# Kernel tuning notes

Hardware: AMD Instinct MI355X
Metric: run time of the kernel (lower is better)

## Reference

```python
import jax, jax.numpy as jnp
import numpy as np

H = 200          # LSTM hidden size
POOL = 16        # maxout pool size


def lstm_step(x, h, c, Wih, Whh, bih, bhh):
    # PyTorch LSTM gate order: i, f, g, o
    gates = x @ Wih.T + h @ Whh.T + bih + bhh  # [4H]
    i, f, g, o = jnp.split(gates, 4)
    i, f, o = jax.nn.sigmoid(i), jax.nn.sigmoid(f), jax.nn.sigmoid(o)
    g = jnp.tanh(g)
    c_new = f * c + i * g
    h_new = o * jnp.tanh(c_new)
    return h_new, c_new


def hmn(U, h, s, e, w1, w2, b2, w3, b3, w4, b4):
    T = U.shape[0]
    r = jnp.tanh(jnp.concatenate([h, s, e]) @ w1.T)                 # [200]
    x = jnp.concatenate([U, jnp.broadcast_to(r, (T, H))], axis=1)    # [T,600]
    m1 = jnp.max((x @ w2.T + b2).reshape(T, POOL, H), axis=1)        # [T,200]
    m2 = jnp.max((m1 @ w3.T + b3).reshape(T, POOL, H), axis=1)       # [T,200]
    a = jnp.max((jnp.concatenate([m1, m2], axis=1) @ w4.T + b4).reshape(T, POOL, 1), axis=1)
    return a[:, 0]                                                   # [T]


def decoder_fwd(U, lstm_Wih, lstm_Whh, lstm_bih, lstm_bhh,
                s_fc1w, s_fc2w, s_fc2b, s_fc3w, s_fc3b, s_fc4w, s_fc4b,
                e_fc1w, e_fc2w, e_fc2b, e_fc3w, e_fc3b, e_fc4w, e_fc4b):
    sp = (s_fc1w, s_fc2w, s_fc2b, s_fc3w, s_fc3b, s_fc4w, s_fc4b)
    ep = (e_fc1w, e_fc2w, e_fc2b, e_fc3w, e_fc3b, e_fc4w, e_fc4b)
    h = jnp.zeros(H, U.dtype)
    c = jnp.zeros(H, U.dtype)
    start = jnp.array(0)
    end = jnp.array(0)

    # iteration 0
    x = jnp.concatenate([U[start], U[end]])
    h, c = lstm_step(x, h, c, lstm_Wih, lstm_Whh, lstm_bih, lstm_bhh)
    alpha = hmn(U, h, U[start], U[end], *sp)
    beta = hmn(U, h, U[start], U[end], *ep)
    start, end = jnp.argmax(alpha), jnp.argmax(beta)
    alphas, betas = [alpha], [beta]
    done = jnp.array(False)

    # iterations 1..3 with early-exit freeze (original breaks when start/end converge)
    for _ in range(3):
        x = jnp.concatenate([U[start], U[end]])
        ch, cc = lstm_step(x, h, c, lstm_Wih, lstm_Whh, lstm_bih, lstm_bhh)
        ca = hmn(U, ch, U[start], U[end], *sp)
        cb = hmn(U, ch, U[start], U[end], *ep)
        ns, ne = jnp.argmax(ca), jnp.argmax(cb)
        alphas.append(jnp.where(done, alphas[-1], ca))
        betas.append(jnp.where(done, betas[-1], cb))
        new_done = done | ((ns == start) & (ne == end))
        h = jnp.where(done, h, ch)
        c = jnp.where(done, c, cc)
        start = jnp.where(done, start, ns)
        end = jnp.where(done, end, ne)
        done = new_done

    return jnp.stack(alphas), jnp.stack(betas)  # each [4, T]


def setup_inputs() -> dict:
    key = jax.random.key(0)
    ks = jax.random.split(key, 24)
    sc = 0.02
    T = 16384
    inp = {
        "U": jax.random.normal(ks[0], (T, 400), dtype=jnp.float32),
        "lstm_Wih": jax.random.normal(ks[1], (4 * H, 800), dtype=jnp.float32) * sc,
        "lstm_Whh": jax.random.normal(ks[2], (4 * H, H), dtype=jnp.float32) * sc,
        "lstm_bih": jnp.zeros(4 * H, jnp.float32),
        "lstm_bhh": jnp.zeros(4 * H, jnp.float32),
    }
    i = 3
    for pre in ("s", "e"):
        inp[pre + "_fc1w"] = jax.random.normal(ks[i], (H, 1000), dtype=jnp.float32) * sc; i += 1
        inp[pre + "_fc2w"] = jax.random.normal(ks[i], (POOL * H, 600), dtype=jnp.float32) * sc; i += 1
        inp[pre + "_fc2b"] = jax.random.normal(ks[i], (POOL * H,), dtype=jnp.float32) * sc; i += 1
        inp[pre + "_fc3w"] = jax.random.normal(ks[i], (POOL * H, H), dtype=jnp.float32) * sc; i += 1
        inp[pre + "_fc3b"] = jax.random.normal(ks[i], (POOL * H,), dtype=jnp.float32) * sc; i += 1
        inp[pre + "_fc4w"] = jax.random.normal(ks[i], (POOL, 2 * H), dtype=jnp.float32) * sc; i += 1
        inp[pre + "_fc4b"] = jax.random.normal(ks[i], (POOL,), dtype=jnp.float32) * sc; i += 1
    return inp


def reference(U, lstm_Wih, lstm_Whh, lstm_bih, lstm_bhh,
              s_fc1w, s_fc2w, s_fc2b, s_fc3w, s_fc3b, s_fc4w, s_fc4b,
              e_fc1w, e_fc2w, e_fc2b, e_fc3w, e_fc3b, e_fc4w, e_fc4b):
    return decoder_fwd(U, lstm_Wih, lstm_Whh, lstm_bih, lstm_bhh,
                       s_fc1w, s_fc2w, s_fc2b, s_fc3w, s_fc3b, s_fc4w, s_fc4b,
                       e_fc1w, e_fc2w, e_fc2b, e_fc3w, e_fc3b, e_fc4w, e_fc4b)
```

## Files before the change

kernel.cpp:

```cpp
#include <hip/hip_runtime.h>
#include <math.h>

#define T_LEN 16384
#define HDIM 200
#define NPOOL 16

typedef __bf16 v8bf __attribute__((ext_vector_type(8)));
typedef float v4f __attribute__((ext_vector_type(4)));

__device__ float g_ca[T_LEN];
__device__ float g_cb[T_LEN];
__device__ float g_rw2s[NPOOL * HDIM];
__device__ float g_rw2e[NPOOL * HDIM];
__device__ float g_gates[4 * HDIM];
__device__ float g_h[HDIM];
__device__ float g_c[HDIM];
__device__ float g_ch[HDIM];
__device__ float g_cc[HDIM];
__device__ float g_rs[HDIM];
__device__ float g_re[HDIM];
__device__ int   g_ctrl[17];
__device__ __align__(16) unsigned short g_Ubf[T_LEN * 400];
__device__ __align__(16) unsigned short g_w2bf[2][3200 * 416];
__device__ __align__(16) unsigned short g_w3bf[2][3200 * 224];
__device__ __align__(16) unsigned short g_w4a[2][16 * 448];
__device__ __align__(16) unsigned short g_m1[2][T_LEN * 224];
__device__ __align__(16) unsigned short g_m2[2][T_LEN * 224];

__device__ inline unsigned short f2bf(float f) {
    unsigned int u = __builtin_bit_cast(unsigned int, f);
    unsigned int r = u + 0x7FFFu + ((u >> 16) & 1u);
    return (unsigned short)(r >> 16);
}
__device__ inline v8bf zero8() {
    return __builtin_bit_cast(v8bf, make_uint4(0u, 0u, 0u, 0u));
}
__device__ inline int clampT(int v) {
    return v < 0 ? 0 : (v >= T_LEN ? T_LEN - 1 : v);
}

__device__ inline void gl_lds16(const unsigned short* g, unsigned short* l) {
    __builtin_amdgcn_global_load_lds(
        (const __attribute__((address_space(1))) unsigned int*)g,
        (__attribute__((address_space(3))) unsigned int*)l,
        16, 0, 0);
}

#define CU_CH   819200
#define C2_CH   166400
#define C3_CH   89600
#define W4A_CH  1792
#define PZ_CH   196608
#define TOT_CH  (CU_CH + 2*C2_CH + 2*C3_CH + W4A_CH + PZ_CH)

__device__ inline void cvt_chunk(const float* __restrict__ src, unsigned short* __restrict__ dst,
                                 int src_stride, int cpr, int ncc, int idx) {
    int r = idx / cpr, c = idx - r * cpr;
    unsigned short o[8] = {0, 0, 0, 0, 0, 0, 0, 0};
    if (c < ncc) {
        const float* s = src + r * src_stride + c * 8;
        float4 f0 = reinterpret_cast<const float4*>(s)[0];
        float4 f1 = reinterpret_cast<const float4*>(s)[1];
        o[0] = f2bf(f0.x); o[1] = f2bf(f0.y); o[2] = f2bf(f0.z); o[3] = f2bf(f0.w);
        o[4] = f2bf(f1.x); o[5] = f2bf(f1.y); o[6] = f2bf(f1.z); o[7] = f2bf(f1.w);
    }
    *reinterpret_cast<uint4*>(dst + r * (cpr * 8) + c * 8) = *reinterpret_cast<uint4*>(o);
}

__global__ void k_cvt_all(const float* __restrict__ U,
                          const float* __restrict__ s_w2, const float* __restrict__ e_w2,
                          const float* __restrict__ s_w3, const float* __restrict__ e_w3,
                          const float* __restrict__ s_w4, const float* __restrict__ e_w4) {
    int i = blockIdx.x * 256 + threadIdx.x;
    if (i < CU_CH) { cvt_chunk(U, g_Ubf, 400, 50, 50, i); return; }
    i -= CU_CH;
    if (i < C2_CH) { cvt_chunk(s_w2, g_w2bf[0], 600, 52, 50, i); return; }
    i -= C2_CH;
    if (i < C2_CH) { cvt_chunk(e_w2, g_w2bf[1], 600, 52, 50, i); return; }
    i -= C2_CH;
    if (i < C3_CH) { cvt_chunk(s_w3, g_w3bf[0], 200, 28, 25, i); return; }
    i -= C3_CH;
    if (i < C3_CH) { cvt_chunk(e_w3, g_w3bf[1], 200, 28, 25, i); return; }
    i -= C3_CH;
    if (i < W4A_CH) {
        int net = i / 896, rem = i - net * 896;
        int r = rem / 56, c = rem - r * 56;
        const float* src = net ? e_w4 : s_w4;
        unsigned short o[8];
#pragma unroll
        for (int j = 0; j < 8; j++) {
            int k = c * 8 + j;
            float v = 0.f;
            if (k < 200) v = src[r * 400 + k];
            else if (k >= 224 && k < 424) v = src[r * 400 + (k - 24)];
            o[j] = f2bf(v);
        }
        *reinterpret_cast<uint4*>(&g_w4a[net][r * 448 + c * 8]) = *reinterpret_cast<uint4*>(o);
        return;
    }
    i -= W4A_CH;
    if (i < PZ_CH) {
        int buf = i / 98304, rem = i - buf * 98304;
        int net = rem / 49152, rem2 = rem - net * 49152;
        int row = rem2 / 3, c = rem2 - row * 3;
        unsigned short* dst = (buf ? g_m2[net] : g_m1[net]) + row * 224 + 200 + c * 8;
        *reinterpret_cast<uint4*>(dst) = make_uint4(0u, 0u, 0u, 0u);
        return;
    }
    i -= PZ_CH;
    if (i < HDIM) { g_h[i] = 0.f; g_c[i] = 0.f; return; }
    i -= HDIM;
    if (i == 0) { g_ctrl[0] = 0; g_ctrl[1] = 0; g_ctrl[2] = 0; }
}

__global__ void k_gates(const float* __restrict__ U,
                        const float* __restrict__ Wih,
                        const float* __restrict__ Whh,
                        const float* __restrict__ bih,
                        const float* __restrict__ bhh,
                        int k) {
    int row = blockIdx.x * 16 + (threadIdx.x >> 4);
    int l = threadIdx.x & 15;
    int start = clampT(g_ctrl[k * 3 + 0]), end = clampT(g_ctrl[k * 3 + 1]);
    float sum = 0.f;
    for (int j = l; j < 800; j += 16) {
        float xv = (j < 400) ? U[start * 400 + j] : U[end * 400 + (j - 400)];
        sum += Wih[row * 800 + j] * xv;
    }
    for (int j = l; j < HDIM; j += 16)
        sum += Whh[row * HDIM + j] * g_h[j];
    for (int off = 8; off > 0; off >>= 1) sum += __shfl_xor(sum, off, 16);
    if (l == 0) g_gates[row] = sum + bih[row] + bhh[row];
}

__global__ void k_r(const float* __restrict__ U,
                    const float* __restrict__ s_w1,
                    const float* __restrict__ e_w1,
                    int k) {
    __shared__ float ch_s[HDIM];
    int t = threadIdx.x;
    if (t < HDIM) {
        float gi = g_gates[t], gf = g_gates[HDIM + t];
        float gg = g_gates[2 * HDIM + t], go = g_gates[3 * HDIM + t];
        float si = 1.f / (1.f + expf(-gi));
        float sf = 1.f / (1.f + expf(-gf));
        float so = 1.f / (1.f + expf(-go));
        float tg = tanhf(gg);
        float cn = sf * g_c[t] + si * tg;
        float hv = so * tanhf(cn);
        ch_s[t] = hv;
        if (blockIdx.x == 0) { g_ch[t] = hv; g_cc[t] = cn; }
    }
    __syncthreads();
    int g = blockIdx.x * 16 + (threadIdx.x >> 4);
    int l = threadIdx.x & 15;
    int net = g / HDIM, i = g % HDIM;
    const float* w1 = net ? e_w1 : s_w1;
    int start = clampT(g_ctrl[k * 3 + 0]), end = clampT(g_ctrl[k * 3 + 1]);
    float sum = 0.f;
    for (int j = l; j < 1000; j += 16) {
        float cv;
        if (j < 200) cv = ch_s[j];
        else if (j < 600) cv = U[start * 400 + (j - 200)];
        else cv = U[end * 400 + (j - 600)];
        sum += w1[i * 1000 + j] * cv;
    }
    for (int off = 8; off > 0; off >>= 1) sum += __shfl_xor(sum, off, 16);
    if (l == 0) { float* out = net ? g_re : g_rs; out[i] = tanhf(sum); }
}

__global__ void k_rw2(const float* __restrict__ s_w2,
                      const float* __restrict__ s_b2,
                      const float* __restrict__ e_w2,
                      const float* __restrict__ e_b2) {
    int g = blockIdx.x * 16 + (threadIdx.x >> 4);
    int l = threadIdx.x & 15;
    int net = g / 3200, n = g % 3200;
    const float* w2 = net ? e_w2 : s_w2;
    const float* b2 = net ? e_b2 : s_b2;
    const float* r = net ? g_re : g_rs;
    float sum = 0.f;
    for (int j = l; j < HDIM; j += 16)
        sum += w2[n * 600 + 400 + j] * r[j];
    for (int off = 8; off > 0; off >>= 1) sum += __shfl_xor(sum, off, 16);
    if (l == 0) { float* out = net ? g_rw2e : g_rw2s; out[n] = sum + b2[n]; }
}

__global__ __launch_bounds__(128, 2) void k_m1() {
    const int bid = blockIdx.x;
    const int net = (bid >> 2) & 1;
    const int r = (bid >> 3) * 4 + (bid & 3);
    const int half = r & 1;
    const int m0 = (r >> 1) * 64;
    const unsigned short* w2 = g_w2bf[net];
    const float* rw2 = net ? g_rw2e : g_rw2s;
    unsigned short* m1o = g_m1[net];
    __shared__ __align__(16) unsigned short Bs[2][6656];
    const int tid = threadIdx.x;
    const int lane = tid & 63, wave = tid >> 6;
    const int q = lane >> 4, col = lane & 15, qo = q * 8;
    const int rowb = m0 + wave * 32;
    const int njt = half ? 6 : 7;
    const int T2 = njt * 16;

    v8bf a1[2][13];
#pragma unroll
    for (int s = 0; s < 2; s++) {
        const unsigned short* ap = g_Ubf + (rowb + s * 16 + col) * 400 + qo;
#pragma unroll
        for (int ks = 0; ks < 13; ks++) {
            if (ks < 12 || q < 2) a1[s][ks] = *reinterpret_cast<const v8bf*>(ap + ks * 32);
            else a1[s][ks] = zero8();
        }
    }
    {
        const unsigned short* gb = w2 + (half * 16 + col) * 416 + qo;
        for (int c = wave; c < 13; c += 2) gl_lds16(gb + c * 32, &Bs[0][c * 512]);
    }
    v4f mx0, mx1;
    for (int t = 0; t < T2; t++) {
        __syncthreads();
        if (t + 1 < T2) {
            int jtn = ((t + 1) >> 4) * 2 + half, pn = (t + 1) & 15;
            int j0n = (jtn < 12) ? jtn * 16 : 184;
            const unsigned short* gb = w2 + (pn * HDIM + j0n + col) * 416 + qo;
            unsigned short* lb = Bs[(t + 1) & 1];
            for (int c = wave; c < 13; c += 2) gl_lds16(gb + c * 32, lb + c * 512);
        }
        const unsigned short* bb = Bs[t & 1];
        int jt = (t >> 4) * 2 + half, p = t & 15;
        int j0 = (jt < 12) ? jt * 16 : 184;
        int n = j0 + col;
        if (p == 0) {
            mx0 = (v4f){-INFINITY, -INFINITY, -INFINITY, -INFINITY};
            mx1 = mx0;
        }
        v4f a00 = {0.f, 0.f, 0.f, 0.f}, a01 = a00, a10 = a00, a11 = a00;
#pragma unroll
        for (int ks = 0; ks < 12; ks += 2) {
            v8bf b0 = *reinterpret_cast<const v8bf*>(&bb[ks * 512 + lane * 8]);
            a00 = __builtin_amdgcn_mfma_f32_16x16x32_bf16(a1[0][ks], b0, a00, 0, 0, 0);
            a10 = __builtin_amdgcn_mfma_f32_16x16x32_bf16(a1[1][ks], b0, a10, 0, 0, 0);
            v8bf b1 = *reinterpret_cast<const v8bf*>(&bb[(ks + 1) * 512 + lane * 8]);
            a01 = __builtin_amdgcn_mfma_f32_16x16x32_bf16(a1[0][ks + 1], b1, a01, 0, 0, 0);
            a11 = __builtin_amdgcn_mfma_f32_16x16x32_bf16(a1[1][ks + 1], b1, a11, 0, 0, 0);
        }
        {
            v8bf b0 = *reinterpret_cast<const v8bf*>(&bb[12 * 512 + lane * 8]);
            a00 = __builtin_amdgcn_mfma_f32_16x16x32_bf16(a1[0][12], b0, a00, 0, 0, 0);
            a10 = __builtin_amdgcn_mfma_f32_16x16x32_bf16(a1[1][12], b0, a10, 0, 0, 0);
        }
        float rv = rw2[p * HDIM + n];
#pragma unroll
        for (int i = 0; i < 4; i++) {
            mx0[i] = fmaxf(mx0[i], a00[i] + a01[i] + rv);
            mx1[i] = fmaxf(mx1[i], a10[i] + a11[i] + rv);
        }
        if (p == 15) {
#pragma unroll
            for (int i = 0; i < 4; i++) {
                m1o[(rowb + q * 4 + i) * 224 + n] = f2bf(mx0[i]);
                m1o[(rowb + 16 + q * 4 + i) * 224 + n] = f2bf(mx1[i]);
            }
        }
    }
}

__global__ __launch_bounds__(128, 2) void k_m2(
    const float* __restrict__ b3s, const float* __restrict__ b3e) {
    const int bid = blockIdx.x;
    const int net = (bid >> 2) & 1;
    const int r = (bid >> 3) * 4 + (bid & 3);
    const int half = r & 1;
    const int m0 = (r >> 1) * 64;
    const unsigned short* w3 = g_w3bf[net];
    const float* b3 = net ? b3e : b3s;
    unsigned short* m2o = g_m2[net];
    __shared__ __align__(16) unsigned short Bs[2][3584];
    const int tid = threadIdx.x;
    const int lane = tid & 63, wave = tid >> 6;
    const int q = lane >> 4, col = lane & 15, qo = q * 8;
    const int rowb = m0 + wave * 32;
    const int njt = half ? 6 : 7;
    const int T2 = njt * 16;

    v8bf a2[2][7];
#pragma unroll
    for (int s = 0; s < 2; s++) {
        const unsigned short* ap = g_m1[net] + (rowb + s * 16 + col) * 224 + qo;
#pragma unroll
        for (int ks = 0; ks < 7; ks++)
            a2[s][ks] = *reinterpret_cast<const v8bf*>(ap + ks * 32);
    }
    {
        const unsigned short* gb = w3 + (half * 16 + col) * 224 + qo;
        for (int c = wave; c < 7; c += 2) gl_lds16(gb + c * 32, &Bs[0][c * 512]);
    }
    v4f mx0, mx1;
    for (int t = 0; t < T2; t++) {
        __syncthreads();
        if (t + 1 < T2) {
            int jtn = ((t + 1) >> 4) * 2 + half, pn = (t + 1) & 15;
            int j0n = (jtn < 12) ? jtn * 16 : 184;
            const unsigned short* gb = w3 + (pn * HDIM + j0n + col) * 224 + qo;
            unsigned short* lb = Bs[(t + 1) & 1];
            for (int c = wave; c < 7; c += 2) gl_lds16(gb + c * 32, lb + c * 512);
        }
        const unsigned short* bb = Bs[t & 1];
        int jt = (t >> 4) * 2 + half, p = t & 15;
        int j0 = (jt < 12) ? jt * 16 : 184;
        int n = j0 + col;
        if (p == 0) {
            mx0 = (v4f){-INFINITY, -INFINITY, -INFINITY, -INFINITY};
            mx1 = mx0;
        }
        v4f a00 = {0.f, 0.f, 0.f, 0.f}, a01 = a00, a10 = a00, a11 = a00;
#pragma unroll
        for (int ks = 0; ks < 6; ks += 2) {
            v8bf b0 = *reinterpret_cast<const v8bf*>(&bb[ks * 512 + lane * 8]);
            a00 = __builtin_amdgcn_mfma_f32_16x16x32_bf16(a2[0][ks], b0, a00, 0, 0, 0);
            a10 = __builtin_amdgcn_mfma_f32_16x16x32_bf16(a2[1][ks], b0, a10, 0, 0, 0);
            v8bf b1 = *reinterpret_cast<const v8bf*>(&bb[(ks + 1) * 512 + lane * 8]);
            a01 = __builtin_amdgcn_mfma_f32_16x16x32_bf16(a2[0][ks + 1], b1, a01, 0, 0, 0);
            a11 = __builtin_amdgcn_mfma_f32_16x16x32_bf16(a2[1][ks + 1], b1, a11, 0, 0, 0);
        }
        {
            v8bf b0 = *reinterpret_cast<const v8bf*>(&bb[6 * 512 + lane * 8]);
            a00 = __builtin_amdgcn_mfma_f32_16x16x32_bf16(a2[0][6], b0, a00, 0, 0, 0);
            a10 = __builtin_amdgcn_mfma_f32_16x16x32_bf16(a2[1][6], b0, a10, 0, 0, 0);
        }
        float bv = b3[p * HDIM + n];
#pragma unroll
        for (int i = 0; i < 4; i++) {
            mx0[i] = fmaxf(mx0[i], a00[i] + a01[i] + bv);
            mx1[i] = fmaxf(mx1[i], a10[i] + a11[i] + bv);
        }
        if (p == 15) {
#pragma unroll
            for (int i = 0; i < 4; i++) {
                m2o[(rowb + q * 4 + i) * 224 + n] = f2bf(mx0[i]);
                m2o[(rowb + 16 + q * 4 + i) * 224 + n] = f2bf(mx1[i]);
            }
        }
    }
}

__global__ __launch_bounds__(128) void k_alpha(
    const float* __restrict__ b4s, const float* __restrict__ b4e) {
    const int bid = blockIdx.x;
    const int net = (bid >> 2) & 1;
    const int m0 = ((bid >> 3) * 4 + (bid & 3)) * 64;
    const unsigned short* w4 = g_w4a[net];
    const float* b4 = net ? b4e : b4s;
    float* outv = net ? g_cb : g_ca;
    const int tid = threadIdx.x;
    const int lane = tid & 63, wave = tid >> 6;
    const int q = lane >> 4, col = lane & 15, qo = q * 8;
    const int rowb = m0 + wave * 32;

    v4f ac0 = {0.f, 0.f, 0.f, 0.f}, ac1 = ac0;
#pragma unroll
    for (int half = 0; half < 2; half++) {
        const unsigned short* src = half ? g_m2[net] : g_m1[net];
#pragma unroll
        for (int ks = 0; ks < 7; ks++) {
            v8bf b = *reinterpret_cast<const v8bf*>(&w4[col * 448 + half * 224 + ks * 32 + qo]);
            v8bf x0 = *reinterpret_cast<const v8bf*>(src + (rowb + col) * 224 + ks * 32 + qo);
            ac0 = __builtin_amdgcn_mfma_f32_16x16x32_bf16(x0, b, ac0, 0, 0, 0);
            v8bf x1 = *reinterpret_cast<const v8bf*>(src + (rowb + 16 + col) * 224 + ks * 32 + qo);
            ac1 = __builtin_amdgcn_mfma_f32_16x16x32_bf16(x1, b, ac1, 0, 0, 0);
        }
    }
    float bbi = b4[col];
#pragma unroll
    for (int s = 0; s < 2; s++) {
        v4f ac = s ? ac1 : ac0;
        float v0 = ac[0] + bbi, v1 = ac[1] + bbi, v2 = ac[2] + bbi, v3 = ac[3] + bbi;
        for (int off = 1; off < 16; off <<= 1) {
            v0 = fmaxf(v0, __shfl_xor(v0, off, 16));
            v1 = fmaxf(v1, __shfl_xor(v1, off, 16));
            v2 = fmaxf(v2, __shfl_xor(v2, off, 16));
            v3 = fmaxf(v3, __shfl_xor(v3, off, 16));
        }
        if (col == 0) {
            const int tb = rowb + s * 16 + q * 4;
            outv[tb + 0] = v0;
            outv[tb + 1] = v1;
            outv[tb + 2] = v2;
            outv[tb + 3] = v3;
        }
    }
}

__global__ void k_commit(int k, float* __restrict__ out) {
    int done = g_ctrl[k * 3 + 2];
    if (blockIdx.x < 128) {
        int is_beta = blockIdx.x >= 64;
        int t = ((int)blockIdx.x & 63) * 256 + threadIdx.x;
        float* row = out + (is_beta ? 4 * T_LEN : 0) + k * T_LEN;
        if (done) row[t] = row[t - T_LEN];
        else row[t] = (is_beta ? g_cb : g_ca)[t];
    } else {
        __shared__ float sv[256];
        __shared__ int si[256];
        int ns = 0, ne = 0;
        for (int which = 0; which < 2; which++) {
            const float* src = which ? g_cb : g_ca;
            float best = -INFINITY;
            int bi = T_LEN - 1;
            for (int t = threadIdx.x; t < T_LEN; t += 256) {
                float v = src[t];
                if (v > best) { best = v; bi = t; }
            }
            sv[threadIdx.x] = best; si[threadIdx.x] = bi;
            __syncthreads();
            for (int s = 128; s > 0; s >>= 1) {
                if (threadIdx.x < s) {
                    float ov = sv[threadIdx.x + s]; int oi = si[threadIdx.x + s];
                    if (ov > sv[threadIdx.x] || (ov == sv[threadIdx.x] && oi < si[threadIdx.x])) {
                        sv[threadIdx.x] = ov; si[threadIdx.x] = oi;
                    }
                }
                __syncthreads();
            }
            if (which == 0) ns = clampT(si[0]); else ne = clampT(si[0]);
            __syncthreads();
        }
        int t = threadIdx.x;
        if (t < HDIM && !done) { g_h[t] = g_ch[t]; g_c[t] = g_cc[t]; }
        if (t == 0) {
            int sp = g_ctrl[k * 3 + 0], ep = g_ctrl[k * 3 + 1];
            if (done) {
                g_ctrl[(k + 1) * 3 + 0] = sp;
                g_ctrl[(k + 1) * 3 + 1] = ep;
                g_ctrl[(k + 1) * 3 + 2] = 1;
            } else {
                g_ctrl[(k + 1) * 3 + 0] = ns;
                g_ctrl[(k + 1) * 3 + 1] = ne;
                g_ctrl[(k + 1) * 3 + 2] = (k == 0) ? 0 : ((ns == sp && ne == ep) ? 1 : 0);
            }
        }
    }
}

extern "C" void kernel_launch(void* const* d_in, const int* in_sizes, int n_in,
                              void* d_out, int out_size, void* d_ws, size_t ws_size,
                              hipStream_t stream) {
    const float* U    = (const float*)d_in[0];
    const float* Wih  = (const float*)d_in[1];
    const float* Whh  = (const float*)d_in[2];
    const float* bih  = (const float*)d_in[3];
    const float* bhh  = (const float*)d_in[4];
    const float* s_w1 = (const float*)d_in[5];
    const float* s_w2 = (const float*)d_in[6];
    const float* s_b2 = (const float*)d_in[7];
    const float* s_w3 = (const float*)d_in[8];
    const float* s_b3 = (const float*)d_in[9];
    const float* s_w4 = (const float*)d_in[10];
    const float* s_b4 = (const float*)d_in[11];
    const float* e_w1 = (const float*)d_in[12];
    const float* e_w2 = (const float*)d_in[13];
    const float* e_b2 = (const float*)d_in[14];
    const float* e_w3 = (const float*)d_in[15];
    const float* e_b3 = (const float*)d_in[16];
    const float* e_w4 = (const float*)d_in[17];
    const float* e_b4 = (const float*)d_in[18];
    float* out = (float*)d_out;
    (void)d_ws; (void)ws_size; (void)in_sizes; (void)n_in; (void)out_size;

    const int cvt_blocks = (TOT_CH + HDIM + 1 + 255) / 256;
    k_cvt_all<<<cvt_blocks, 256, 0, stream>>>(U, s_w2, e_w2, s_w3, e_w3, s_w4, e_w4);

    for (int k = 0; k < 4; k++) {
        k_gates<<<50, 256, 0, stream>>>(U, Wih, Whh, bih, bhh, k);
        k_r<<<25, 256, 0, stream>>>(U, s_w1, e_w1, k);
        k_rw2<<<400, 256, 0, stream>>>(s_w2, s_b2, e_w2, e_b2);
        k_m1<<<1024, 128, 0, stream>>>();
        k_m2<<<1024, 128, 0, stream>>>(s_b3, e_b3);
        k_alpha<<<512, 128, 0, stream>>>(s_b4, e_b4);
        k_commit<<<129, 256, 0, stream>>>(k, out);
    }
}
```

Before: 1.307 ms.

## Widen m1/m2 blocks to four waves sharing B tiles; vectorize GEMV kernels

The m1 and m2 maxout GEMM kernels now run with 256 threads covering 128 rows per block. Four waves share each LDS-staged weight tile, which halves the number of blocks and the redundant weight traffic into LDS. The small GEMV kernels (gates, r, rw2) switch to float4 loads with a dot4 helper, and the buffers they read get 16-byte alignment. The larger blocks reduce the number of blocks and may change occupancy, and float4 reads rely on the row strides being multiples of four.

```diff
diff --git a/kernel.cpp b/kernel.cpp
--- a/kernel.cpp
+++ b/kernel.cpp
@@ -12,13 +12,13 @@
 __device__ float g_cb[T_LEN];
 __device__ float g_rw2s[NPOOL * HDIM];
 __device__ float g_rw2e[NPOOL * HDIM];
-__device__ float g_gates[4 * HDIM];
-__device__ float g_h[HDIM];
-__device__ float g_c[HDIM];
-__device__ float g_ch[HDIM];
-__device__ float g_cc[HDIM];
-__device__ float g_rs[HDIM];
-__device__ float g_re[HDIM];
+__device__ __align__(16) float g_gates[4 * HDIM];
+__device__ __align__(16) float g_h[HDIM];
+__device__ __align__(16) float g_c[HDIM];
+__device__ __align__(16) float g_ch[HDIM];
+__device__ __align__(16) float g_cc[HDIM];
+__device__ __align__(16) float g_rs[HDIM];
+__device__ __align__(16) float g_re[HDIM];
 __device__ int   g_ctrl[17];
 __device__ __align__(16) unsigned short g_Ubf[T_LEN * 400];
 __device__ __align__(16) unsigned short g_w2bf[2][3200 * 416];
@@ -37,6 +37,9 @@
 }
 __device__ inline int clampT(int v) {
     return v < 0 ? 0 : (v >= T_LEN ? T_LEN - 1 : v);
+}
+__device__ inline float dot4(float4 a, float4 b) {
+    return fmaf(a.x, b.x, fmaf(a.y, b.y, fmaf(a.z, b.z, a.w * b.w)));
 }
 
 __device__ inline void gl_lds16(const unsigned short* g, unsigned short* l) {
@@ -122,13 +125,18 @@
     int row = blockIdx.x * 16 + (threadIdx.x >> 4);
     int l = threadIdx.x & 15;
     int start = clampT(g_ctrl[k * 3 + 0]), end = clampT(g_ctrl[k * 3 + 1]);
+    const float4* W4 = reinterpret_cast<const float4*>(Wih) + row * 200;
+    const float4* Us = reinterpret_cast<const float4*>(U + start * 400);
+    const float4* Ue = reinterpret_cast<const float4*>(U + end * 400);
     float sum = 0.f;
-    for (int j = l; j < 800; j += 16) {
-        float xv = (j < 400) ? U[start * 400 + j] : U[end * 400 + (j - 400)];
-        sum += Wih[row * 800 + j] * xv;
-    }
-    for (int j = l; j < HDIM; j += 16)
-        sum += Whh[row * HDIM + j] * g_h[j];
+    for (int c = l; c < 200; c += 16) {
+        float4 xv = (c < 100) ? Us[c] : Ue[c - 100];
+        sum += dot4(W4[c], xv);
+    }
+    const float4* Wh4 = reinterpret_cast<const float4*>(Whh) + row * 50;
+    const float4* h4 = reinterpret_cast<const float4*>(g_h);
+    for (int c = l; c < 50; c += 16)
+        sum += dot4(Wh4[c], h4[c]);
     for (int off = 8; off > 0; off >>= 1) sum += __shfl_xor(sum, off, 16);
     if (l == 0) g_gates[row] = sum + bih[row] + bhh[row];
 }
@@ -137,7 +145,7 @@
                     const float* __restrict__ s_w1,
                     const float* __restrict__ e_w1,
                     int k) {
-    __shared__ float ch_s[HDIM];
+    __shared__ __align__(16) float ch_s[HDIM];
     int t = threadIdx.x;
     if (t < HDIM) {
         float gi = g_gates[t], gf = g_gates[HDIM + t];
@@ -157,13 +165,17 @@
     int net = g / HDIM, i = g % HDIM;
     const float* w1 = net ? e_w1 : s_w1;
     int start = clampT(g_ctrl[k * 3 + 0]), end = clampT(g_ctrl[k * 3 + 1]);
+    const float4* w14 = reinterpret_cast<const float4*>(w1) + i * 250;
+    const float4* c4 = reinterpret_cast<const float4*>(ch_s);
+    const float4* Us = reinterpret_cast<const float4*>(U + start * 400);
+    const float4* Ue = reinterpret_cast<const float4*>(U + end * 400);
     float sum = 0.f;
-    for (int j = l; j < 1000; j += 16) {
-        float cv;
-        if (j < 200) cv = ch_s[j];
-        else if (j < 600) cv = U[start * 400 + (j - 200)];
-        else cv = U[end * 400 + (j - 600)];
-        sum += w1[i * 1000 + j] * cv;
+    for (int c = l; c < 250; c += 16) {
+        float4 cv;
+        if (c < 50) cv = c4[c];
+        else if (c < 150) cv = Us[c - 50];
+        else cv = Ue[c - 150];
+        sum += dot4(w14[c], cv);
     }
     for (int off = 8; off > 0; off >>= 1) sum += __shfl_xor(sum, off, 16);
     if (l == 0) { float* out = net ? g_re : g_rs; out[i] = tanhf(sum); }
@@ -178,20 +190,21 @@
     int net = g / 3200, n = g % 3200;
     const float* w2 = net ? e_w2 : s_w2;
     const float* b2 = net ? e_b2 : s_b2;
-    const float* r = net ? g_re : g_rs;
+    const float4* r4 = reinterpret_cast<const float4*>(net ? g_re : g_rs);
+    const float4* w24 = reinterpret_cast<const float4*>(w2) + n * 150 + 100;
     float sum = 0.f;
-    for (int j = l; j < HDIM; j += 16)
-        sum += w2[n * 600 + 400 + j] * r[j];
+    for (int c = l; c < 50; c += 16)
+        sum += dot4(w24[c], r4[c]);
     for (int off = 8; off > 0; off >>= 1) sum += __shfl_xor(sum, off, 16);
     if (l == 0) { float* out = net ? g_rw2e : g_rw2s; out[n] = sum + b2[n]; }
 }
 
-__global__ __launch_bounds__(128, 2) void k_m1() {
+__global__ __launch_bounds__(256, 2) void k_m1() {
     const int bid = blockIdx.x;
     const int net = (bid >> 2) & 1;
     const int r = (bid >> 3) * 4 + (bid & 3);
     const int half = r & 1;
-    const int m0 = (r >> 1) * 64;
+    const int m0 = (r >> 1) * 128;
     const unsigned short* w2 = g_w2bf[net];
     const float* rw2 = net ? g_rw2e : g_rw2s;
     unsigned short* m1o = g_m1[net];
@@ -215,7 +228,7 @@
     }
     {
         const unsigned short* gb = w2 + (half * 16 + col) * 416 + qo;
-        for (int c = wave; c < 13; c += 2) gl_lds16(gb + c * 32, &Bs[0][c * 512]);
+        for (int c = wave; c < 13; c += 4) gl_lds16(gb + c * 32, &Bs[0][c * 512]);
     }
     v4f mx0, mx1;
     for (int t = 0; t < T2; t++) {
@@ -225,7 +238,7 @@
             int j0n = (jtn < 12) ? jtn * 16 : 184;
             const unsigned short* gb = w2 + (pn * HDIM + j0n + col) * 416 + qo;
             unsigned short* lb = Bs[(t + 1) & 1];
-            for (int c = wave; c < 13; c += 2) gl_lds16(gb + c * 32, lb + c * 512);
+            for (int c = wave; c < 13; c += 4) gl_lds16(gb + c * 32, lb + c * 512);
         }
         const unsigned short* bb = Bs[t & 1];
         int jt = (t >> 4) * 2 + half, p = t & 15;
@@ -266,13 +279,13 @@
     }
 }
 
-__global__ __launch_bounds__(128, 2) void k_m2(
+__global__ __launch_bounds__(256, 2) void k_m2(
     const float* __restrict__ b3s, const float* __restrict__ b3e) {
     const int bid = blockIdx.x;
     const int net = (bid >> 2) & 1;
     const int r = (bid >> 3) * 4 + (bid & 3);
     const int half = r & 1;
-    const int m0 = (r >> 1) * 64;
+    const int m0 = (r >> 1) * 128;
     const unsigned short* w3 = g_w3bf[net];
     const float* b3 = net ? b3e : b3s;
     unsigned short* m2o = g_m2[net];
@@ -294,7 +307,7 @@
     }
     {
         const unsigned short* gb = w3 + (half * 16 + col) * 224 + qo;
-        for (int c = wave; c < 7; c += 2) gl_lds16(gb + c * 32, &Bs[0][c * 512]);
+        for (int c = wave; c < 7; c += 4) gl_lds16(gb + c * 32, &Bs[0][c * 512]);
     }
     v4f mx0, mx1;
     for (int t = 0; t < T2; t++) {
@@ -304,7 +317,7 @@
             int j0n = (jtn < 12) ? jtn * 16 : 184;
             const unsigned short* gb = w3 + (pn * HDIM + j0n + col) * 224 + qo;
             unsigned short* lb = Bs[(t + 1) & 1];
-            for (int c = wave; c < 7; c += 2) gl_lds16(gb + c * 32, lb + c * 512);
+            for (int c = wave; c < 7; c += 4) gl_lds16(gb + c * 32, lb + c * 512);
         }
         const unsigned short* bb = Bs[t & 1];
         int jt = (t >> 4) * 2 + half, p = t & 15;
@@ -475,8 +488,8 @@
         k_gates<<<50, 256, 0, stream>>>(U, Wih, Whh, bih, bhh, k);
         k_r<<<25, 256, 0, stream>>>(U, s_w1, e_w1, k);
         k_rw2<<<400, 256, 0, stream>>>(s_w2, s_b2, e_w2, e_b2);
-        k_m1<<<1024, 128, 0, stream>>>();
-        k_m2<<<1024, 128, 0, stream>>>(s_b3, e_b3);
+        k_m1<<<512, 256, 0, stream>>>();
+        k_m2<<<512, 256, 0, stream>>>(s_b3, e_b3);
         k_alpha<<<512, 128, 0, stream>>>(s_b4, e_b4);
         k_commit<<<129, 256, 0, stream>>>(k, out);
     }
```

Result: faster. 1.087 ms (-16.8%).
